# Kernel tuning notes

Hardware: AMD Instinct MI355X
Metric: run time of the kernel (lower is better)

Reference implementation:

```python
import jax, jax.numpy as jnp
import numpy as np

N_NODES = 100000
N_EDGES = 1200000


def gcn_conv(h, W, b, src, dst, n_nodes):
    """PyG GCNConv: h' = D^-1/2 (A+I) D^-1/2 (h W) + b, with self-loops."""
    h = h @ W  # [N, out]
    # degree on A + I (count of incoming edges at dst, plus self-loop)
    deg = jnp.zeros((n_nodes,), h.dtype).at[dst].add(1.0) + 1.0
    dis = jax.lax.rsqrt(deg)  # deg^-1/2, deg >= 1 so safe
    norm = dis[src] * dis[dst]  # [E]
    out = jnp.zeros_like(h).at[dst].add(norm[:, None] * h[src])
    out = out + (1.0 / deg)[:, None] * h  # self-loop term: dis_i^2 * h_i
    return out + b


def global_features(x, T_norm):
    # matches compute_global_features; torch uses .item() so these are constants
    n_comp = jnp.sum(x[:, 2])
    n_AND = jnp.sum(x[:, 3])
    n_OR = jnp.sum(x[:, 4])
    mask = (x[:, 2] == 1.0).astype(x.dtype)
    msum = jnp.sum(mask)
    safe = jnp.maximum(msum, 1.0)
    avg_lambda = jnp.where(msum > 0, jnp.sum(x[:, 0] * mask) / safe, 0.0)
    avg_mu = jnp.where(msum > 0, jnp.sum(x[:, 1] * mask) / safe, 0.0)
    depth = n_AND + n_OR
    g = jnp.stack([n_comp, n_AND, n_OR, depth, avg_lambda, avg_mu, T_norm])[None, :]
    return jax.lax.stop_gradient(g)


def setup_inputs() -> dict:
    key = jax.random.key(0)
    ks = jax.random.split(key, 8)
    x = jax.random.normal(ks[0], (N_NODES, 5), jnp.float32)
    edge_index = jax.random.randint(ks[1], (2, N_EDGES), 0, N_NODES, jnp.int64)
    sc = lambda f: 1.0 / np.sqrt(f)
    return {
        "x": x,
        "edge_index": edge_index,
        "W1": jax.random.normal(ks[2], (5, 64), jnp.float32) * sc(5),
        "b1": jnp.zeros((64,), jnp.float32),
        "W2": jax.random.normal(ks[3], (64, 64), jnp.float32) * sc(64),
        "b2": jnp.zeros((64,), jnp.float32),
        "Wp1": jax.random.normal(ks[4], (71, 32), jnp.float32) * sc(71),
        "bp1": jnp.zeros((32,), jnp.float32),
        "Wp2": jax.random.normal(ks[5], (32, 2), jnp.float32) * sc(32),
        "bp2": jnp.zeros((2,), jnp.float32),
        "T": 100,
        "T_max": 500,
    }


def reference(x, edge_index, W1, b1, W2, b2, Wp1, bp1, Wp2, bp2, T, T_max):
    src, dst = edge_index[0], edge_index[1]
    n = x.shape[0]
    h = jax.nn.relu(gcn_conv(x, W1, b1, src, dst, n))
    h = jax.nn.relu(gcn_conv(h, W2, b2, src, dst, n))
    embedding = jnp.mean(h, axis=0, keepdims=True)  # global_mean_pool, single graph
    T_norm = jnp.asarray(T, x.dtype) / jnp.asarray(T_max, x.dtype)
    g = global_features(x, T_norm)
    e = jnp.concatenate([embedding, g], axis=1)  # [1, 71]
    raw = jax.nn.relu(e @ Wp1 + bp1) @ Wp2 + bp2  # [1, 2]
    return 2.0 + jax.nn.sigmoid(raw) * 4.0
```

## Files before the change

### kernel.cpp

```cpp
#include <hip/hip_runtime.h>
#include <hip/hip_bf16.h>

#define N_NODES_C 100000
#define N_EDGES_C 1200000
#define NB2 98
#define SUBCAP2 1792

typedef unsigned int uint32;
typedef __attribute__((ext_vector_type(8))) short bf16x8;
typedef __attribute__((ext_vector_type(4))) float f32x4;

__device__ __forceinline__ float bf_lo(uint32 u) { return __uint_as_float(u << 16); }
__device__ __forceinline__ float bf_hi(uint32 u) { return __uint_as_float(u & 0xffff0000u); }
__device__ __forceinline__ uint32 bf16r(float f) {
    uint32 u = __float_as_uint(f);
    return (u + 0x7fffu + ((u >> 16) & 1u)) >> 16;
}
__device__ __forceinline__ uint32 pack2(float lo, float hi) {
    return bf16r(lo) | (bf16r(hi) << 16);
}

__global__ void bucket_kernel(const int4* __restrict__ src4, const int4* __restrict__ dst4,
                              int* __restrict__ bcnt, int2* __restrict__ bedges, int nE4) {
    __shared__ int cntL[NB2];
    __shared__ int baseL[NB2];
    int tid = threadIdx.x;
    int i = blockIdx.x * 256 + tid;
    int sub = blockIdx.x & 7;
    for (int t = tid; t < NB2; t += 256) cntL[t] = 0;
    __syncthreads();
    int4 s4 = make_int4(0, 0, 0, 0), d4 = make_int4(0, 0, 0, 0);
    int b0 = 0, b1 = 0, b2 = 0, b3 = 0;
    bool act = i < nE4;
    if (act) {
        s4 = src4[i];
        d4 = dst4[i];
        b0 = d4.x >> 10; b1 = d4.y >> 10; b2 = d4.z >> 10; b3 = d4.w >> 10;
        atomicAdd(&cntL[b0], 1); atomicAdd(&cntL[b1], 1);
        atomicAdd(&cntL[b2], 1); atomicAdd(&cntL[b3], 1);
    }
    __syncthreads();
    for (int t = tid; t < NB2; t += 256) {
        int n = cntL[t];
        baseL[t] = n ? atomicAdd(&bcnt[sub * NB2 + t], n) : 0;
    }
    __syncthreads();
    for (int t = tid; t < NB2; t += 256) cntL[t] = 0;
    __syncthreads();
    if (act) {
        int o, slot;
        o = atomicAdd(&cntL[b0], 1); slot = baseL[b0] + o;
        if (slot < SUBCAP2) bedges[((size_t)b0 * 8 + sub) * SUBCAP2 + slot] = make_int2(s4.x, d4.x);
        o = atomicAdd(&cntL[b1], 1); slot = baseL[b1] + o;
        if (slot < SUBCAP2) bedges[((size_t)b1 * 8 + sub) * SUBCAP2 + slot] = make_int2(s4.y, d4.y);
        o = atomicAdd(&cntL[b2], 1); slot = baseL[b2] + o;
        if (slot < SUBCAP2) bedges[((size_t)b2 * 8 + sub) * SUBCAP2 + slot] = make_int2(s4.z, d4.z);
        o = atomicAdd(&cntL[b3], 1); slot = baseL[b3] + o;
        if (slot < SUBCAP2) bedges[((size_t)b3 * 8 + sub) * SUBCAP2 + slot] = make_int2(s4.w, d4.w);
    }
}

__global__ void cnt2_kernel(const int2* __restrict__ bedges, const int* __restrict__ bcnt,
                            int* __restrict__ cnt, int nN) {
    __shared__ int lc[1024];
    __shared__ int ln[8];
    int b = blockIdx.x;
    int tid = threadIdx.x;
    lc[tid] = 0;
    if (tid < 8) ln[tid] = min(bcnt[tid * NB2 + b], SUBCAP2);
    __syncthreads();
    const int2* be = bedges + (size_t)b * 8 * SUBCAP2;
#pragma unroll
    for (int s = 0; s < 8; ++s) {
        int n = ln[s];
        const int2* bs = be + s * SUBCAP2;
        for (int i = tid; i < n; i += 1024) atomicAdd(&lc[bs[i].y & 1023], 1);
    }
    __syncthreads();
    int node = b * 1024 + tid;
    if (node < nN) cnt[node] = lc[tid];
}

__global__ void bsum_kernel(const int* __restrict__ cnt, int* __restrict__ bsum, int nN) {
    __shared__ int sm[256];
    int tid = threadIdx.x;
    int base = blockIdx.x * 1024 + tid * 4;
    int s = 0;
#pragma unroll
    for (int k = 0; k < 4; ++k)
        if (base + k < nN) s += cnt[base + k];
    sm[tid] = s;
    __syncthreads();
    for (int off = 128; off > 0; off >>= 1) {
        if (tid < off) sm[tid] += sm[tid + off];
        __syncthreads();
    }
    if (tid == 0) bsum[blockIdx.x] = sm[0];
}

__global__ void bscan_kernel(const int* __restrict__ bsum, int* __restrict__ boff, int nb) {
    __shared__ int sm[128];
    int tid = threadIdx.x;
    sm[tid] = (tid < nb) ? bsum[tid] : 0;
    __syncthreads();
    for (int off = 1; off < 128; off <<= 1) {
        int t = (tid >= off) ? sm[tid - off] : 0;
        __syncthreads();
        sm[tid] += t;
        __syncthreads();
    }
    if (tid < nb) boff[tid] = (tid ? sm[tid - 1] : 0);
}

__global__ void scan_block_kernel(const int* __restrict__ cnt, const int* __restrict__ boff,
                                  int* __restrict__ rowptr, float* __restrict__ dis, int nN) {
    __shared__ int sm[256];
    int tid = threadIdx.x;
    int base = blockIdx.x * 1024 + tid * 4;
    int v0 = 0, v1 = 0, v2 = 0, v3 = 0;
    if (base + 0 < nN) v0 = cnt[base + 0];
    if (base + 1 < nN) v1 = cnt[base + 1];
    if (base + 2 < nN) v2 = cnt[base + 2];
    if (base + 3 < nN) v3 = cnt[base + 3];
    int tsum = v0 + v1 + v2 + v3;
    sm[tid] = tsum;
    __syncthreads();
    for (int off = 1; off < 256; off <<= 1) {
        int t = (tid >= off) ? sm[tid - off] : 0;
        __syncthreads();
        sm[tid] += t;
        __syncthreads();
    }
    int excl = (tid ? sm[tid - 1] : 0) + boff[blockIdx.x];
    if (base + 0 <= nN) rowptr[base + 0] = excl;
    if (base + 1 <= nN) rowptr[base + 1] = excl + v0;
    if (base + 2 <= nN) rowptr[base + 2] = excl + v0 + v1;
    if (base + 3 <= nN) rowptr[base + 3] = excl + v0 + v1 + v2;
    if (base + 0 < nN) dis[base + 0] = rsqrtf((float)(v0 + 1));
    if (base + 1 < nN) dis[base + 1] = rsqrtf((float)(v1 + 1));
    if (base + 2 < nN) dis[base + 2] = rsqrtf((float)(v2 + 1));
    if (base + 3 < nN) dis[base + 3] = rsqrtf((float)(v3 + 1));
}

__global__ void bin2_kernel(const int2* __restrict__ bedges, const int* __restrict__ bcnt,
                            const int* __restrict__ rowptr, int* __restrict__ csr_src) {
    __shared__ int lfill[1024];
    __shared__ int ln[8];
    int b = blockIdx.x;
    int tid = threadIdx.x;
    lfill[tid] = 0;
    if (tid < 8) ln[tid] = min(bcnt[tid * NB2 + b], SUBCAP2);
    __syncthreads();
    const int2* be = bedges + (size_t)b * 8 * SUBCAP2;
#pragma unroll
    for (int s = 0; s < 8; ++s) {
        int n = ln[s];
        const int2* bs = be + s * SUBCAP2;
        for (int i = tid; i < n; i += 1024) {
            int2 ed = bs[i];
            int slot = rowptr[ed.y] + atomicAdd(&lfill[ed.y & 1023], 1);
            csr_src[slot] = ed.x;
        }
    }
}

__global__ void lin1_kernel(const float* __restrict__ x, const float* __restrict__ W1,
                            const float* __restrict__ dis, uint32* __restrict__ hlin, int nN) {
    __shared__ float Ws[320];
    int tid = threadIdx.x;
    if (tid < 256) Ws[tid] = W1[tid];
    if (tid < 64)  Ws[256 + tid] = W1[256 + tid];
    __syncthreads();
    int l = tid & 31;
    int sub = tid >> 5;
    for (int node = blockIdx.x * 8 + sub; node < nN; node += gridDim.x * 8) {
        const float* xr = x + node * 5;
        float x0 = xr[0], x1 = xr[1], x2 = xr[2], x3 = xr[3], x4 = xr[4];
        float dn = dis[node];
        int j0 = 2 * l, j1 = 2 * l + 1;
        float a = x0 * Ws[j0] + x1 * Ws[64 + j0] + x2 * Ws[128 + j0]
                + x3 * Ws[192 + j0] + x4 * Ws[256 + j0];
        float b = x0 * Ws[j1] + x1 * Ws[64 + j1] + x2 * Ws[128 + j1]
                + x3 * Ws[192 + j1] + x4 * Ws[256 + j1];
        hlin[node * 32 + l] = pack2(a * dn, b * dn);
    }
}

template <bool EPI>
__global__ void gather_kernel(const int* __restrict__ rowptr, const int* __restrict__ csr_src,
                              const uint4* __restrict__ hin, const float* __restrict__ bias,
                              uint4* __restrict__ hout, int nN) {
    int tid = threadIdx.x;
    int lane = tid & 63;
    int wv = tid >> 6;
    int g = lane >> 3;
    int l = lane & 7;
    float bb0 = 0, bb1 = 0, bb2 = 0, bb3 = 0, bb4 = 0, bb5 = 0, bb6 = 0, bb7 = 0;
    if (EPI) {
        const float* bp = bias + 8 * l;
        bb0 = bp[0]; bb1 = bp[1]; bb2 = bp[2]; bb3 = bp[3];
        bb4 = bp[4]; bb5 = bp[5]; bb6 = bp[6]; bb7 = bp[7];
    }
    int stride = gridDim.x * 32;
    for (int node = blockIdx.x * 32 + wv * 8 + g; node < nN; node += stride) {
        int e0 = rowptr[node];
        int e1 = rowptr[node + 1];
        float a0 = 0, a1 = 0, a2 = 0, a3 = 0, a4 = 0, a5 = 0, a6 = 0, a7 = 0;
        int e = e0;
        for (; e + 2 <= e1; e += 2) {
            int s0 = csr_src[e];
            int s1 = csr_src[e + 1];
            uint4 h0 = hin[(size_t)s0 * 8 + l];
            uint4 h1 = hin[(size_t)s1 * 8 + l];
            a0 += bf_lo(h0.x) + bf_lo(h1.x); a1 += bf_hi(h0.x) + bf_hi(h1.x);
            a2 += bf_lo(h0.y) + bf_lo(h1.y); a3 += bf_hi(h0.y) + bf_hi(h1.y);
            a4 += bf_lo(h0.z) + bf_lo(h1.z); a5 += bf_hi(h0.z) + bf_hi(h1.z);
            a6 += bf_lo(h0.w) + bf_lo(h1.w); a7 += bf_hi(h0.w) + bf_hi(h1.w);
        }
        if (e < e1) {
            int s0 = csr_src[e];
            uint4 h0 = hin[(size_t)s0 * 8 + l];
            a0 += bf_lo(h0.x); a1 += bf_hi(h0.x);
            a2 += bf_lo(h0.y); a3 += bf_hi(h0.y);
            a4 += bf_lo(h0.z); a5 += bf_hi(h0.z);
            a6 += bf_lo(h0.w); a7 += bf_hi(h0.w);
        }
        float dn = rsqrtf((float)(e1 - e0 + 1));
        uint4 hs = hin[(size_t)node * 8 + l];
        a0 = (a0 + bf_lo(hs.x)) * dn; a1 = (a1 + bf_hi(hs.x)) * dn;
        a2 = (a2 + bf_lo(hs.y)) * dn; a3 = (a3 + bf_hi(hs.y)) * dn;
        a4 = (a4 + bf_lo(hs.z)) * dn; a5 = (a5 + bf_hi(hs.z)) * dn;
        a6 = (a6 + bf_lo(hs.w)) * dn; a7 = (a7 + bf_hi(hs.w)) * dn;
        if (EPI) {
            a0 = fmaxf(a0 + bb0, 0.0f) * dn; a1 = fmaxf(a1 + bb1, 0.0f) * dn;
            a2 = fmaxf(a2 + bb2, 0.0f) * dn; a3 = fmaxf(a3 + bb3, 0.0f) * dn;
            a4 = fmaxf(a4 + bb4, 0.0f) * dn; a5 = fmaxf(a5 + bb5, 0.0f) * dn;
            a6 = fmaxf(a6 + bb6, 0.0f) * dn; a7 = fmaxf(a7 + bb7, 0.0f) * dn;
        }
        hout[(size_t)node * 8 + l] = make_uint4(pack2(a0, a1), pack2(a2, a3),
                                                pack2(a4, a5), pack2(a6, a7));
    }
}

__global__ void lin2pool_kernel(const uint2* __restrict__ z2, const float* __restrict__ W2,
                                const float* __restrict__ b2, float* __restrict__ colsumB,
                                int nTiles) {
    int tid = threadIdx.x;
    int lane = tid & 63;
    int wv = tid >> 6;
    int l16 = lane & 15;
    int kg = lane >> 4;

    bf16x8 Bf[2][4];
#pragma unroll
    for (int ks = 0; ks < 2; ++ks)
#pragma unroll
        for (int t = 0; t < 4; ++t) {
            bf16x8 bb;
#pragma unroll
            for (int r = 0; r < 8; ++r) {
                int k = ks * 32 + kg * 8 + r;
                bb[r] = (short)bf16r(W2[k * 64 + t * 16 + l16]);
            }
            Bf[ks][t] = bb;
        }
    float bbias[4];
#pragma unroll
    for (int t = 0; t < 4; ++t) bbias[t] = b2[t * 16 + l16];

    float colacc[4][4];
#pragma unroll
    for (int t = 0; t < 4; ++t)
#pragma unroll
        for (int r = 0; r < 4; ++r) colacc[t][r] = 0.0f;

    for (int tile = blockIdx.x * 4 + wv; tile < nTiles; tile += gridDim.x * 4) {
        int nodeBase = tile * 16;
        const uint4* zrow = (const uint4*)(z2 + (size_t)(nodeBase + l16) * 16);
        uint4 A0u = zrow[kg];
        uint4 A1u = zrow[4 + kg];
        union { uint4 u; bf16x8 b; } c0, c1;
        c0.u = A0u; c1.u = A1u;
        f32x4 acc0 = {0, 0, 0, 0}, acc1 = {0, 0, 0, 0}, acc2 = {0, 0, 0, 0}, acc3 = {0, 0, 0, 0};
        acc0 = __builtin_amdgcn_mfma_f32_16x16x32_bf16(c0.b, Bf[0][0], acc0, 0, 0, 0);
        acc1 = __builtin_amdgcn_mfma_f32_16x16x32_bf16(c0.b, Bf[0][1], acc1, 0, 0, 0);
        acc2 = __builtin_amdgcn_mfma_f32_16x16x32_bf16(c0.b, Bf[0][2], acc2, 0, 0, 0);
        acc3 = __builtin_amdgcn_mfma_f32_16x16x32_bf16(c0.b, Bf[0][3], acc3, 0, 0, 0);
        acc0 = __builtin_amdgcn_mfma_f32_16x16x32_bf16(c1.b, Bf[1][0], acc0, 0, 0, 0);
        acc1 = __builtin_amdgcn_mfma_f32_16x16x32_bf16(c1.b, Bf[1][1], acc1, 0, 0, 0);
        acc2 = __builtin_amdgcn_mfma_f32_16x16x32_bf16(c1.b, Bf[1][2], acc2, 0, 0, 0);
        acc3 = __builtin_amdgcn_mfma_f32_16x16x32_bf16(c1.b, Bf[1][3], acc3, 0, 0, 0);
#pragma unroll
        for (int r = 0; r < 4; ++r) {
            colacc[0][r] += fmaxf(acc0[r] + bbias[0], 0.0f);
            colacc[1][r] += fmaxf(acc1[r] + bbias[1], 0.0f);
            colacc[2][r] += fmaxf(acc2[r] + bbias[2], 0.0f);
            colacc[3][r] += fmaxf(acc3[r] + bbias[3], 0.0f);
        }
    }
    float s[4];
#pragma unroll
    for (int t = 0; t < 4; ++t) {
        s[t] = colacc[t][0] + colacc[t][1] + colacc[t][2] + colacc[t][3];
        s[t] += __shfl_down(s[t], 32);
        s[t] += __shfl_down(s[t], 16);
    }
    __shared__ float sm[4][64];
    if (lane < 16) {
#pragma unroll
        for (int t = 0; t < 4; ++t) sm[wv][t * 16 + lane] = s[t];
    }
    __syncthreads();
    if (tid < 64) {
        float v = sm[0][tid] + sm[1][tid] + sm[2][tid] + sm[3][tid];
        atomicAdd(&colsumB[(blockIdx.x & 15) * 64 + tid], v);
    }
}

__global__ void gfeat_kernel(const float* __restrict__ x, float* __restrict__ gsB, int nN) {
    int tid = threadIdx.x;
    int i = blockIdx.x * 256 + tid;
    float s0 = 0, s1 = 0, s2 = 0, s3 = 0, s4 = 0, s5 = 0;
    if (i < nN) {
        const float* xr = x + i * 5;
        float x0 = xr[0], x1 = xr[1], x2 = xr[2], x3 = xr[3], x4 = xr[4];
        float m = (x2 == 1.0f) ? 1.0f : 0.0f;
        s0 = x0 * m; s1 = x1 * m; s2 = x2; s3 = x3; s4 = x4; s5 = m;
    }
#pragma unroll
    for (int off = 32; off > 0; off >>= 1) {
        s0 += __shfl_down(s0, off);
        s1 += __shfl_down(s1, off);
        s2 += __shfl_down(s2, off);
        s3 += __shfl_down(s3, off);
        s4 += __shfl_down(s4, off);
        s5 += __shfl_down(s5, off);
    }
    __shared__ float smg[4][6];
    if ((tid & 63) == 0) {
        int w = tid >> 6;
        smg[w][0] = s0; smg[w][1] = s1; smg[w][2] = s2;
        smg[w][3] = s3; smg[w][4] = s4; smg[w][5] = s5;
    }
    __syncthreads();
    if (tid < 6) {
        float s = smg[0][tid] + smg[1][tid] + smg[2][tid] + smg[3][tid];
        atomicAdd(&gsB[(blockIdx.x & 15) * 16 + tid], s);
    }
}

__global__ void head_kernel(const float* __restrict__ colsumB, const float* __restrict__ gsB,
                            const float* __restrict__ Wp1, const float* __restrict__ bp1,
                            const float* __restrict__ Wp2, const float* __restrict__ bp2,
                            const int* __restrict__ T, const int* __restrict__ Tmax,
                            float* __restrict__ out) {
    __shared__ float e[71];
    __shared__ float gsum[6];
    __shared__ float hid[32];
    int tid = threadIdx.x;
    if (tid < 64) {
        float s = 0.0f;
#pragma unroll
        for (int r = 0; r < 16; ++r) s += colsumB[r * 64 + tid];
        e[tid] = s * (1.0f / (float)N_NODES_C);
    } else if (tid < 70) {
        int k = tid - 64;
        float s = 0.0f;
#pragma unroll
        for (int r = 0; r < 16; ++r) s += gsB[r * 16 + k];
        gsum[k] = s;
    }
    __syncthreads();
    if (tid == 0) {
        e[64] = gsum[2];
        e[65] = gsum[3];
        e[66] = gsum[4];
        e[67] = gsum[3] + gsum[4];
        float m = gsum[5];
        e[68] = (m > 0.0f) ? gsum[0] / fmaxf(m, 1.0f) : 0.0f;
        e[69] = (m > 0.0f) ? gsum[1] / fmaxf(m, 1.0f) : 0.0f;
        e[70] = (float)T[0] / (float)Tmax[0];
    }
    __syncthreads();
    if (tid < 32) {
        float acc = bp1[tid];
        for (int i = 0; i < 71; ++i) acc += e[i] * Wp1[i * 32 + tid];
        hid[tid] = fmaxf(acc, 0.0f);
    }
    __syncthreads();
    if (tid < 2) {
        float acc = bp2[tid];
        for (int k = 0; k < 32; ++k) acc += hid[k] * Wp2[k * 2 + tid];
        out[tid] = 2.0f + 4.0f / (1.0f + expf(-acc));
    }
}

extern "C" void kernel_launch(void* const* d_in, const int* in_sizes, int n_in,
                              void* d_out, int out_size, void* d_ws, size_t ws_size,
                              hipStream_t stream) {
    const float* x    = (const float*)d_in[0];
    const int*   ei   = (const int*)d_in[1];
    const float* W1   = (const float*)d_in[2];
    const float* b1   = (const float*)d_in[3];
    const float* W2   = (const float*)d_in[4];
    const float* b2   = (const float*)d_in[5];
    const float* Wp1  = (const float*)d_in[6];
    const float* bp1  = (const float*)d_in[7];
    const float* Wp2  = (const float*)d_in[8];
    const float* bp2  = (const float*)d_in[9];
    const int*   T    = (const int*)d_in[10];
    const int*   Tmax = (const int*)d_in[11];
    float* out = (float*)d_out;

    const int nN = N_NODES_C;
    const int nE = N_EDGES_C;
    const int* src = ei;
    const int* dst = ei + nE;

    char* ws = (char*)d_ws;
    int*    bcnt    = (int*)   (ws + 0);
    float*  colsumB = (float*) (ws + 3136);
    float*  gsB     = (float*) (ws + 7232);
    int*    bsum    = (int*)   (ws + 8256);
    int*    boff    = (int*)   (ws + 8768);
    int*    cnt     = (int*)   (ws + 9280);
    int*    rowptr  = (int*)   (ws + 409280);
    float*  dis     = (float*) (ws + 809296);
    int*    csr_src = (int*)   (ws + 1209296);
    int2*   bedges  = (int2*)  (ws + 6009296);
    uint32* hlin1   = (uint32*)(ws + 17248720);
    uint32* h1      = (uint32*)(ws + 30048720);
    uint32* z2      = (uint32*)(ws + 42848720);

    hipMemsetAsync(ws, 0, 8256, stream);

    const int nb = (nN + 1023) / 1024;

    bucket_kernel<<<(nE / 4 + 255) / 256, 256, 0, stream>>>(
        (const int4*)src, (const int4*)dst, bcnt, bedges, nE / 4);
    cnt2_kernel<<<NB2, 1024, 0, stream>>>(bedges, bcnt, cnt, nN);
    bsum_kernel<<<nb, 256, 0, stream>>>(cnt, bsum, nN);
    bscan_kernel<<<1, 128, 0, stream>>>(bsum, boff, nb);
    scan_block_kernel<<<nb, 256, 0, stream>>>(cnt, boff, rowptr, dis, nN);
    bin2_kernel<<<NB2, 1024, 0, stream>>>(bedges, bcnt, rowptr, csr_src);

    lin1_kernel<<<1024, 256, 0, stream>>>(x, W1, dis, hlin1, nN);
    gather_kernel<true><<<2048, 256, 0, stream>>>(rowptr, csr_src, (const uint4*)hlin1, b1,
                                                  (uint4*)h1, nN);

    gather_kernel<false><<<2048, 256, 0, stream>>>(rowptr, csr_src, (const uint4*)h1, nullptr,
                                                   (uint4*)z2, nN);
    lin2pool_kernel<<<512, 256, 0, stream>>>((const uint2*)z2, W2, b2, colsumB, nN / 16);

    gfeat_kernel<<<(nN + 255) / 256, 256, 0, stream>>>(x, gsB, nN);

    head_kernel<<<1, 128, 0, stream>>>(colsumB, gsB, Wp1, bp1, Wp2, bp2, T, Tmax, out);
}
```

Before: 222.6 us.

## Store gathered node features in fp8 and pack bucketed edges into 32-bit words

Layer-1 linear output and layer-1 aggregated features are now stored as fp8 (e4m3) instead of bf16, which halves the bytes read per edge in both gather passes. Bucketed edges are packed into one 32-bit word holding a 17-bit source and a 10-bit local destination, halving the scratch traffic in the binning kernels. The risk is reduced numerical precision from fp8, and the packing assumes node ids fit in 17 bits.

```diff
diff --git a/kernel.cpp b/kernel.cpp
--- a/kernel.cpp
+++ b/kernel.cpp
@@ -9,6 +9,7 @@
 typedef unsigned int uint32;
 typedef __attribute__((ext_vector_type(8))) short bf16x8;
 typedef __attribute__((ext_vector_type(4))) float f32x4;
+typedef __attribute__((ext_vector_type(2))) float f32x2;
 
 __device__ __forceinline__ float bf_lo(uint32 u) { return __uint_as_float(u << 16); }
 __device__ __forceinline__ float bf_hi(uint32 u) { return __uint_as_float(u & 0xffff0000u); }
@@ -21,7 +22,7 @@
 }
 
 __global__ void bucket_kernel(const int4* __restrict__ src4, const int4* __restrict__ dst4,
-                              int* __restrict__ bcnt, int2* __restrict__ bedges, int nE4) {
+                              int* __restrict__ bcnt, uint32* __restrict__ bedges, int nE4) {
     __shared__ int cntL[NB2];
     __shared__ int baseL[NB2];
     int tid = threadIdx.x;
@@ -50,17 +51,25 @@
     if (act) {
         int o, slot;
         o = atomicAdd(&cntL[b0], 1); slot = baseL[b0] + o;
-        if (slot < SUBCAP2) bedges[((size_t)b0 * 8 + sub) * SUBCAP2 + slot] = make_int2(s4.x, d4.x);
+        if (slot < SUBCAP2)
+            bedges[((size_t)b0 * 8 + sub) * SUBCAP2 + slot] =
+                (uint32)s4.x | ((uint32)(d4.x & 1023) << 17);
         o = atomicAdd(&cntL[b1], 1); slot = baseL[b1] + o;
-        if (slot < SUBCAP2) bedges[((size_t)b1 * 8 + sub) * SUBCAP2 + slot] = make_int2(s4.y, d4.y);
+        if (slot < SUBCAP2)
+            bedges[((size_t)b1 * 8 + sub) * SUBCAP2 + slot] =
+                (uint32)s4.y | ((uint32)(d4.y & 1023) << 17);
         o = atomicAdd(&cntL[b2], 1); slot = baseL[b2] + o;
-        if (slot < SUBCAP2) bedges[((size_t)b2 * 8 + sub) * SUBCAP2 + slot] = make_int2(s4.z, d4.z);
+        if (slot < SUBCAP2)
+            bedges[((size_t)b2 * 8 + sub) * SUBCAP2 + slot] =
+                (uint32)s4.z | ((uint32)(d4.z & 1023) << 17);
         o = atomicAdd(&cntL[b3], 1); slot = baseL[b3] + o;
-        if (slot < SUBCAP2) bedges[((size_t)b3 * 8 + sub) * SUBCAP2 + slot] = make_int2(s4.w, d4.w);
-    }
-}
-
-__global__ void cnt2_kernel(const int2* __restrict__ bedges, const int* __restrict__ bcnt,
+        if (slot < SUBCAP2)
+            bedges[((size_t)b3 * 8 + sub) * SUBCAP2 + slot] =
+                (uint32)s4.w | ((uint32)(d4.w & 1023) << 17);
+    }
+}
+
+__global__ void cnt2_kernel(const uint32* __restrict__ bedges, const int* __restrict__ bcnt,
                             int* __restrict__ cnt, int nN) {
     __shared__ int lc[1024];
     __shared__ int ln[8];
@@ -69,12 +78,12 @@
     lc[tid] = 0;
     if (tid < 8) ln[tid] = min(bcnt[tid * NB2 + b], SUBCAP2);
     __syncthreads();
-    const int2* be = bedges + (size_t)b * 8 * SUBCAP2;
+    const uint32* be = bedges + (size_t)b * 8 * SUBCAP2;
 #pragma unroll
     for (int s = 0; s < 8; ++s) {
         int n = ln[s];
-        const int2* bs = be + s * SUBCAP2;
-        for (int i = tid; i < n; i += 1024) atomicAdd(&lc[bs[i].y & 1023], 1);
+        const uint32* bs = be + s * SUBCAP2;
+        for (int i = tid; i < n; i += 1024) atomicAdd(&lc[bs[i] >> 17], 1);
     }
     __syncthreads();
     int node = b * 1024 + tid;
@@ -142,7 +151,7 @@
     if (base + 3 < nN) dis[base + 3] = rsqrtf((float)(v3 + 1));
 }
 
-__global__ void bin2_kernel(const int2* __restrict__ bedges, const int* __restrict__ bcnt,
+__global__ void bin2_kernel(const uint32* __restrict__ bedges, const int* __restrict__ bcnt,
                             const int* __restrict__ rowptr, int* __restrict__ csr_src) {
     __shared__ int lfill[1024];
     __shared__ int ln[8];
@@ -151,15 +160,17 @@
     lfill[tid] = 0;
     if (tid < 8) ln[tid] = min(bcnt[tid * NB2 + b], SUBCAP2);
     __syncthreads();
-    const int2* be = bedges + (size_t)b * 8 * SUBCAP2;
+    const uint32* be = bedges + (size_t)b * 8 * SUBCAP2;
+    int nodeBase = b << 10;
 #pragma unroll
     for (int s = 0; s < 8; ++s) {
         int n = ln[s];
-        const int2* bs = be + s * SUBCAP2;
+        const uint32* bs = be + s * SUBCAP2;
         for (int i = tid; i < n; i += 1024) {
-            int2 ed = bs[i];
-            int slot = rowptr[ed.y] + atomicAdd(&lfill[ed.y & 1023], 1);
-            csr_src[slot] = ed.x;
+            uint32 ed = bs[i];
+            int dlow = ed >> 17;
+            int slot = rowptr[nodeBase + dlow] + atomicAdd(&lfill[dlow], 1);
+            csr_src[slot] = ed & 0x1FFFF;
         }
     }
 }
@@ -171,25 +182,28 @@
     if (tid < 256) Ws[tid] = W1[tid];
     if (tid < 64)  Ws[256 + tid] = W1[256 + tid];
     __syncthreads();
-    int l = tid & 31;
-    int sub = tid >> 5;
-    for (int node = blockIdx.x * 8 + sub; node < nN; node += gridDim.x * 8) {
+    int q = tid & 15;
+    int sub = tid >> 4;
+    for (int node = blockIdx.x * 16 + sub; node < nN; node += gridDim.x * 16) {
         const float* xr = x + node * 5;
         float x0 = xr[0], x1 = xr[1], x2 = xr[2], x3 = xr[3], x4 = xr[4];
         float dn = dis[node];
-        int j0 = 2 * l, j1 = 2 * l + 1;
-        float a = x0 * Ws[j0] + x1 * Ws[64 + j0] + x2 * Ws[128 + j0]
-                + x3 * Ws[192 + j0] + x4 * Ws[256 + j0];
-        float b = x0 * Ws[j1] + x1 * Ws[64 + j1] + x2 * Ws[128 + j1]
-                + x3 * Ws[192 + j1] + x4 * Ws[256 + j1];
-        hlin[node * 32 + l] = pack2(a * dn, b * dn);
+        int j = 4 * q;
+        float a0 = x0 * Ws[j+0] + x1 * Ws[64+j+0] + x2 * Ws[128+j+0] + x3 * Ws[192+j+0] + x4 * Ws[256+j+0];
+        float a1 = x0 * Ws[j+1] + x1 * Ws[64+j+1] + x2 * Ws[128+j+1] + x3 * Ws[192+j+1] + x4 * Ws[256+j+1];
+        float a2 = x0 * Ws[j+2] + x1 * Ws[64+j+2] + x2 * Ws[128+j+2] + x3 * Ws[192+j+2] + x4 * Ws[256+j+2];
+        float a3 = x0 * Ws[j+3] + x1 * Ws[64+j+3] + x2 * Ws[128+j+3] + x3 * Ws[192+j+3] + x4 * Ws[256+j+3];
+        uint32 w = 0;
+        w = __builtin_amdgcn_cvt_pk_fp8_f32(a0 * dn, a1 * dn, w, 0);
+        w = __builtin_amdgcn_cvt_pk_fp8_f32(a2 * dn, a3 * dn, w, 1);
+        hlin[node * 16 + q] = w;
     }
 }
 
 template <bool EPI>
 __global__ void gather_kernel(const int* __restrict__ rowptr, const int* __restrict__ csr_src,
-                              const uint4* __restrict__ hin, const float* __restrict__ bias,
-                              uint4* __restrict__ hout, int nN) {
+                              const uint2* __restrict__ hin, const float* __restrict__ bias,
+                              void* __restrict__ hout, int nN) {
     int tid = threadIdx.x;
     int lane = tid & 63;
     int wv = tid >> 6;
@@ -210,35 +224,58 @@
         for (; e + 2 <= e1; e += 2) {
             int s0 = csr_src[e];
             int s1 = csr_src[e + 1];
-            uint4 h0 = hin[(size_t)s0 * 8 + l];
-            uint4 h1 = hin[(size_t)s1 * 8 + l];
-            a0 += bf_lo(h0.x) + bf_lo(h1.x); a1 += bf_hi(h0.x) + bf_hi(h1.x);
-            a2 += bf_lo(h0.y) + bf_lo(h1.y); a3 += bf_hi(h0.y) + bf_hi(h1.y);
-            a4 += bf_lo(h0.z) + bf_lo(h1.z); a5 += bf_hi(h0.z) + bf_hi(h1.z);
-            a6 += bf_lo(h0.w) + bf_lo(h1.w); a7 += bf_hi(h0.w) + bf_hi(h1.w);
+            uint2 h0 = hin[(size_t)s0 * 8 + l];
+            uint2 h1 = hin[(size_t)s1 * 8 + l];
+            f32x2 p0 = __builtin_amdgcn_cvt_pk_f32_fp8(h0.x, 0);
+            f32x2 p1 = __builtin_amdgcn_cvt_pk_f32_fp8(h0.x, 1);
+            f32x2 p2 = __builtin_amdgcn_cvt_pk_f32_fp8(h0.y, 0);
+            f32x2 p3 = __builtin_amdgcn_cvt_pk_f32_fp8(h0.y, 1);
+            f32x2 q0 = __builtin_amdgcn_cvt_pk_f32_fp8(h1.x, 0);
+            f32x2 q1 = __builtin_amdgcn_cvt_pk_f32_fp8(h1.x, 1);
+            f32x2 q2 = __builtin_amdgcn_cvt_pk_f32_fp8(h1.y, 0);
+            f32x2 q3 = __builtin_amdgcn_cvt_pk_f32_fp8(h1.y, 1);
+            a0 += p0.x + q0.x; a1 += p0.y + q0.y;
+            a2 += p1.x + q1.x; a3 += p1.y + q1.y;
+            a4 += p2.x + q2.x; a5 += p2.y + q2.y;
+            a6 += p3.x + q3.x; a7 += p3.y + q3.y;
         }
         if (e < e1) {
             int s0 = csr_src[e];
-            uint4 h0 = hin[(size_t)s0 * 8 + l];
-            a0 += bf_lo(h0.x); a1 += bf_hi(h0.x);
-            a2 += bf_lo(h0.y); a3 += bf_hi(h0.y);
-            a4 += bf_lo(h0.z); a5 += bf_hi(h0.z);
-            a6 += bf_lo(h0.w); a7 += bf_hi(h0.w);
+            uint2 h0 = hin[(size_t)s0 * 8 + l];
+            f32x2 p0 = __builtin_amdgcn_cvt_pk_f32_fp8(h0.x, 0);
+            f32x2 p1 = __builtin_amdgcn_cvt_pk_f32_fp8(h0.x, 1);
+            f32x2 p2 = __builtin_amdgcn_cvt_pk_f32_fp8(h0.y, 0);
+            f32x2 p3 = __builtin_amdgcn_cvt_pk_f32_fp8(h0.y, 1);
+            a0 += p0.x; a1 += p0.y; a2 += p1.x; a3 += p1.y;
+            a4 += p2.x; a5 += p2.y; a6 += p3.x; a7 += p3.y;
         }
         float dn = rsqrtf((float)(e1 - e0 + 1));
-        uint4 hs = hin[(size_t)node * 8 + l];
-        a0 = (a0 + bf_lo(hs.x)) * dn; a1 = (a1 + bf_hi(hs.x)) * dn;
-        a2 = (a2 + bf_lo(hs.y)) * dn; a3 = (a3 + bf_hi(hs.y)) * dn;
-        a4 = (a4 + bf_lo(hs.z)) * dn; a5 = (a5 + bf_hi(hs.z)) * dn;
-        a6 = (a6 + bf_lo(hs.w)) * dn; a7 = (a7 + bf_hi(hs.w)) * dn;
+        uint2 hs = hin[(size_t)node * 8 + l];
+        {
+            f32x2 p0 = __builtin_amdgcn_cvt_pk_f32_fp8(hs.x, 0);
+            f32x2 p1 = __builtin_amdgcn_cvt_pk_f32_fp8(hs.x, 1);
+            f32x2 p2 = __builtin_amdgcn_cvt_pk_f32_fp8(hs.y, 0);
+            f32x2 p3 = __builtin_amdgcn_cvt_pk_f32_fp8(hs.y, 1);
+            a0 = (a0 + p0.x) * dn; a1 = (a1 + p0.y) * dn;
+            a2 = (a2 + p1.x) * dn; a3 = (a3 + p1.y) * dn;
+            a4 = (a4 + p2.x) * dn; a5 = (a5 + p2.y) * dn;
+            a6 = (a6 + p3.x) * dn; a7 = (a7 + p3.y) * dn;
+        }
         if (EPI) {
             a0 = fmaxf(a0 + bb0, 0.0f) * dn; a1 = fmaxf(a1 + bb1, 0.0f) * dn;
             a2 = fmaxf(a2 + bb2, 0.0f) * dn; a3 = fmaxf(a3 + bb3, 0.0f) * dn;
             a4 = fmaxf(a4 + bb4, 0.0f) * dn; a5 = fmaxf(a5 + bb5, 0.0f) * dn;
             a6 = fmaxf(a6 + bb6, 0.0f) * dn; a7 = fmaxf(a7 + bb7, 0.0f) * dn;
-        }
-        hout[(size_t)node * 8 + l] = make_uint4(pack2(a0, a1), pack2(a2, a3),
-                                                pack2(a4, a5), pack2(a6, a7));
+            uint32 w0 = 0, w1 = 0;
+            w0 = __builtin_amdgcn_cvt_pk_fp8_f32(a0, a1, w0, 0);
+            w0 = __builtin_amdgcn_cvt_pk_fp8_f32(a2, a3, w0, 1);
+            w1 = __builtin_amdgcn_cvt_pk_fp8_f32(a4, a5, w1, 0);
+            w1 = __builtin_amdgcn_cvt_pk_fp8_f32(a6, a7, w1, 1);
+            ((uint2*)hout)[(size_t)node * 8 + l] = make_uint2(w0, w1);
+        } else {
+            ((uint4*)hout)[(size_t)node * 8 + l] = make_uint4(pack2(a0, a1), pack2(a2, a3),
+                                                              pack2(a4, a5), pack2(a6, a7));
+        }
     }
 }
 
@@ -427,10 +464,10 @@
     int*    rowptr  = (int*)   (ws + 409280);
     float*  dis     = (float*) (ws + 809296);
     int*    csr_src = (int*)   (ws + 1209296);
-    int2*   bedges  = (int2*)  (ws + 6009296);
-    uint32* hlin1   = (uint32*)(ws + 17248720);
-    uint32* h1      = (uint32*)(ws + 30048720);
-    uint32* z2      = (uint32*)(ws + 42848720);
+    uint32* bedges  = (uint32*)(ws + 6009296);
+    uint32* hlin1   = (uint32*)(ws + 11629008);
+    uint32* h1      = (uint32*)(ws + 18029008);
+    uint32* z2      = (uint32*)(ws + 24429008);
 
     hipMemsetAsync(ws, 0, 8256, stream);
 
@@ -445,11 +482,11 @@
     bin2_kernel<<<NB2, 1024, 0, stream>>>(bedges, bcnt, rowptr, csr_src);
 
     lin1_kernel<<<1024, 256, 0, stream>>>(x, W1, dis, hlin1, nN);
-    gather_kernel<true><<<2048, 256, 0, stream>>>(rowptr, csr_src, (const uint4*)hlin1, b1,
-                                                  (uint4*)h1, nN);
-
-    gather_kernel<false><<<2048, 256, 0, stream>>>(rowptr, csr_src, (const uint4*)h1, nullptr,
-                                                   (uint4*)z2, nN);
+    gather_kernel<true><<<2048, 256, 0, stream>>>(rowptr, csr_src, (const uint2*)hlin1, b1,
+                                                  (void*)h1, nN);
+
+    gather_kernel<false><<<2048, 256, 0, stream>>>(rowptr, csr_src, (const uint2*)h1, nullptr,
+                                                   (void*)z2, nN);
     lin2pool_kernel<<<512, 256, 0, stream>>>((const uint2*)z2, W2, b2, colsumB, nN / 16);
 
     gfeat_kernel<<<(nN + 255) / 256, 256, 0, stream>>>(x, gsB, nN);
```

Measured after the change: 189.4 us. 1.18x faster.
